# Optimization experiments

Hardware: AMD Instinct MI355X
Metric: run time of the kernel (lower is better)

## Reference

```python
import jax, jax.numpy as jnp
import numpy as np

ELU = jax.nn.elu
RELU = jax.nn.relu


def _mlp(x, W0, b0, Wh, bh, Wo, bo, act):
    # first hidden layer, stacked middle hidden layers, linear output layer
    h = act(x @ W0 + b0)
    for i in range(Wh.shape[0]):
        h = act(h @ Wh[i] + bh[i])
    return h @ Wo + bo


def _gru_layer(x_seq, h0, Wi, Wh, bi, bh):
    # torch nn.GRU gate math. x_seq: (T,B,I), h0: (B,H)
    xi = x_seq @ Wi.T + bi  # (T,B,3H) precomputed input projection

    def step(h, xt):
        hh = h @ Wh.T + bh
        xr, xz, xn = jnp.split(xt, 3, -1)
        hr, hz, hn = jnp.split(hh, 3, -1)
        r = jax.nn.sigmoid(xr + hr)
        z = jax.nn.sigmoid(xz + hz)
        n = jnp.tanh(xn + r * hn)
        hnew = (1.0 - z) * n + z * h
        return hnew, hnew

    hT, ys = jax.lax.scan(step, h0, xi)
    return ys, hT


def setup_inputs() -> dict:
    key = jax.random.key(0)
    ks = iter(jax.random.split(key, 64))
    B, T = 1024, 512
    S, SE, OE, GH = 4, 16, 16, 16
    OBJ_N, NULL_N, NOBJ = 3, 4, 7
    p = lambda *shape: jax.random.normal(next(ks), shape, jnp.float32) * 0.1
    return dict(
        envs=jax.random.normal(next(ks), (B, 9), jnp.float32),
        states=jax.random.normal(next(ks), (B, T, S), jnp.float32),
        # state embedder: 4 -> [16]*4 -> 16 (relu)
        se_W0=p(S, SE), se_b0=p(SE), se_Wh=p(3, SE, SE), se_bh=p(3, SE), se_Wo=p(SE, SE), se_bo=p(SE),
        # per-object embedders: 3 -> [16]*4 -> 16 (elu), stacked over 3 objects
        oe_W0=p(OBJ_N, 3, OE), oe_b0=p(OBJ_N, OE), oe_Wh=p(OBJ_N, 3, OE, OE), oe_bh=p(OBJ_N, 3, OE),
        oe_Wo=p(OBJ_N, OE, OE), oe_bo=p(OBJ_N, OE),
        null_embed=jax.random.uniform(next(ks), (NULL_N, OE), jnp.float32),
        init_gru_h=jax.random.uniform(next(ks), (2, GH), jnp.float32),
        # attention-score mlp: 32 -> [16]*3 -> 1 (elu)
        att_W0=p(SE + OE, 16), att_b0=p(16), att_Wh=p(2, 16, 16), att_bh=p(2, 16), att_Wo=p(16, 1), att_bo=p(1),
        # GRU: 2 layers, input 128, hidden 16
        gru0_Wi=p(3 * GH, SE + OE * NOBJ), gru0_Wh=p(3 * GH, GH), gru0_bi=p(3 * GH), gru0_bh=p(3 * GH),
        gru1_Wi=p(3 * GH, GH), gru1_Wh=p(3 * GH, GH), gru1_bi=p(3 * GH), gru1_bh=p(3 * GH),
        # relation MLPs: 32 -> [8]*2 -> 8 (elu), stacked over 7 slots
        rel_W0=p(NOBJ, GH + OE, 8), rel_b0=p(NOBJ, 8), rel_Wh=p(NOBJ, 1, 8, 8), rel_bh=p(NOBJ, 1, 8),
        rel_Wo=p(NOBJ, 8, 8), rel_bo=p(NOBJ, 8),
        # final mlp: 72 -> [4]*2 -> 4 (elu)
        fin_W0=p(GH + 8 * NOBJ, S), fin_b0=p(S), fin_Wh=p(1, S, S), fin_bh=p(1, S), fin_Wo=p(S, S), fin_bo=p(S),
        predict_t=0,
    )


def reference(envs, states, se_W0, se_b0, se_Wh, se_bh, se_Wo, se_bo,
              oe_W0, oe_b0, oe_Wh, oe_bh, oe_Wo, oe_bo,
              null_embed, init_gru_h,
              att_W0, att_b0, att_Wh, att_bh, att_Wo, att_bo,
              gru0_Wi, gru0_Wh, gru0_bi, gru0_bh, gru1_Wi, gru1_Wh, gru1_bi, gru1_bh,
              rel_W0, rel_b0, rel_Wh, rel_bh, rel_Wo, rel_bo,
              fin_W0, fin_b0, fin_Wh, fin_bh, fin_Wo, fin_bo,
              predict_t):
    B = envs.shape[0]
    T = states.shape[1]
    NOBJ = rel_W0.shape[0]  # 7 = obj_n + nullobj_n
    OE = null_embed.shape[1]

    # per-object embeddings: split envs into obj_n chunks, run per-slot MLPs (grouped via vmap)
    env_objs = envs.reshape(B, 3, 3).transpose(1, 0, 2)  # (3,B,3)
    obj_real = jax.vmap(lambda x, W0, b0, Wh, bh, Wo, bo: _mlp(x, W0, b0, Wh, bh, Wo, bo, ELU))(
        env_objs, oe_W0, oe_b0, oe_Wh, oe_bh, oe_Wo, oe_bo)  # (3,B,16)
    obj_null = jnp.broadcast_to(null_embed[:, None, :], (null_embed.shape[0], B, OE))  # (4,B,16)
    obj_embd = jnp.concatenate([obj_real, obj_null], 0)           # (7,B,16)
    obj_t = jnp.broadcast_to(obj_embd[:, None], (NOBJ, T, B, OE))  # (7,T,B,16)

    # state embedding over the full sequence (time-major like torch GRU)
    se = _mlp(states.transpose(1, 0, 2), se_W0, se_b0, se_Wh, se_bh, se_Wo, se_bo, RELU)  # (T,B,16)

    # attention scores per object slot
    def score_fn(emb):
        xin = jnp.concatenate([se, emb], -1)  # (T,B,32)
        return _mlp(xin, att_W0, att_b0, att_Wh, att_bh, att_Wo, att_bo, ELU)[..., 0]
    scores = jax.vmap(score_fn)(obj_t)  # (7,T,B)
    # PermuteLayer reverses the slot ordering before softmax over slots
    col_scores = jax.nn.softmax(jnp.flip(scores, 0), axis=0)  # (7,T,B)

    # GRU over [state_emb ; all obj embeds]
    gru_in = jnp.concatenate([se, jnp.moveaxis(obj_t, 0, 2).reshape(T, B, NOBJ * OE)], -1)  # (T,B,128)
    h0 = jnp.broadcast_to(init_gru_h[:, None, :], (2, B, init_gru_h.shape[1]))
    y0, _ = _gru_layer(gru_in, h0[0], gru0_Wi, gru0_Wh, gru0_bi, gru0_bh)
    gru_out, _ = _gru_layer(y0, h0[1], gru1_Wi, gru1_Wh, gru1_bi, gru1_bh)  # (T,B,16)

    # per-slot relation MLPs weighted by attention
    def rel_fn(emb, w, W0, b0, Wh, bh, Wo, bo):
        xin = jnp.concatenate([gru_out, emb], -1)  # (T,B,32)
        r = _mlp(xin, W0, b0, Wh, bh, Wo, bo, ELU)  # (T,B,8)
        return r * w[..., None]
    weighted = jax.vmap(rel_fn)(obj_t, col_scores, rel_W0, rel_b0, rel_Wh, rel_bh, rel_Wo, rel_bo)  # (7,T,B,8)

    final_in = jnp.concatenate([gru_out, jnp.moveaxis(weighted, 0, 2).reshape(T, B, -1)], -1)  # (T,B,72)
    out = _mlp(final_in, fin_W0, fin_b0, fin_Wh, fin_bh, fin_Wo, fin_bo, ELU)  # (T,B,4)
    return out.transpose(1, 0, 2)  # (B,T,4)
```

## Files before the change

kernel.cpp:

```cpp
#include <hip/hip_runtime.h>
#include <hip/hip_bf16.h>
#include <hip/hip_fp16.h>
#include <stdint.h>

#define TLEN 512
#define TCW 48
#define NCHK 11
__device__ __forceinline__ int csize(int i){ return (i == 10) ? 32 : 48; }

typedef unsigned short u16;
typedef unsigned int u32;

__device__ __forceinline__ float b2f(u16 u){ union{u32 i; float f;} v; v.i = ((u32)u)<<16; return v.f; }
__device__ __forceinline__ u16 f2bf(float f){
    union{float f; u32 i;} v; v.f = f;
    u32 b = v.i; b += 0x7fffu + ((b>>16)&1u);
    return (u16)(b>>16);
}
__device__ __forceinline__ float fexp2(float x){ return __builtin_amdgcn_exp2f(x); }
__device__ __forceinline__ float frcp(float x){ return __builtin_amdgcn_rcpf(x); }
#define LOG2E 1.4426950408889634f
__device__ __forceinline__ float elu_f(float x){ return x > 0.f ? x : fexp2(x*LOG2E) - 1.f; }
__device__ __forceinline__ float sigm(float x){ return frcp(1.f + fexp2(-LOG2E*x)); }
__device__ __forceinline__ float tanh_f(float x){ return 1.f - 2.f*frcp(1.f + fexp2((2.f*LOG2E)*x)); }

__device__ __forceinline__ float ldg(const void* p, int i, bool F){
    return F ? ((const float*)p)[i] : b2f(((const u16*)p)[i]);
}

__device__ void fill(float* dst, const void* src, int n, int tid, int nt, bool F){
    for (int i = tid; i < n; i += nt) dst[i] = ldg(src, i, F);
}
__device__ void fillS(float* dst, const void* src, int R, int C, int stride, int tid, int nt, bool F){
    for (int i = tid; i < R*C; i += nt){ int r = i / C, c = i % C; dst[i] = ldg(src, r*stride + c, F); }
}
__device__ void fillT(float* dst, const void* src, int K, int I, int stride, int tid, int nt, bool F){
    for (int idx = tid; idx < K*I; idx += nt){ int i = idx / K, k = idx % K; dst[idx] = ldg(src, k*stride + i, F); }
}

__global__ __launch_bounds__(256,1) void fused(
    const void* envs, const void* states,
    const void* se_W0, const void* se_b0, const void* se_Wh, const void* se_bh, const void* se_Wo, const void* se_bo,
    const void* oe_W0, const void* oe_b0, const void* oe_Wh, const void* oe_bh, const void* oe_Wo, const void* oe_bo,
    const void* null_embed, const void* init_h,
    const void* att_W0, const void* att_b0, const void* att_Wh, const void* att_bh, const void* att_Wo, const void* att_bo,
    const void* gru0_Wi, const void* gru0_Wh, const void* gru0_bi, const void* gru0_bh,
    const void* gru1_Wi, const void* gru1_Wh, const void* gru1_bi, const void* gru1_bh,
    const void* rel_W0, const void* rel_b0, const void* rel_Wh, const void* rel_bh, const void* rel_Wo, const void* rel_bo,
    const void* fin_W0, const void* fin_b0, const void* fin_Wh, const void* fin_bh, const void* fin_Wo, const void* fin_bo,
    void* out)
{
    __shared__ float sW0T[64], sb0[16], sWhT[768], sbh[48], sWoT[256], sbo[16];
    __shared__ float aW0T[256], aWhT[512], abh[32], aWo[16], abo_s[1];
    __shared__ float wi0se[768];
    __shared__ float rW0T[896], rWhT[448], rbh[56], rWoT[448], rbo[56];
    __shared__ float fW0T[288], fb0[4], fWhT[16], fbh[4], fWoT[16], fbo[4];
    __shared__ float E_att[448], E_rel[224], base_xi[192];
    __shared__ float gW0[768], gWi1[768], gWh1[768];
    __shared__ float g0bhn[16], g1bi48[48], g1bh48[48];
    __shared__ float scbuf[1728];
    __shared__ float uni[13632];
    __shared__ int s_isf32;

    const int tid = threadIdx.x, nt = 256;
    const int blk = blockIdx.x;
    const int wid = tid >> 6, ln = tid & 63;

    _Float16* bufA = (_Float16*)(uni);
    _Float16* bufB = (_Float16*)(uni + 4608);
    _Float16* gruA = (_Float16*)(uni + 9216);
    _Float16* gruB = (_Float16*)(uni + 10752);
    _Float16* cscA = (_Float16*)(uni + 12288);
    _Float16* cscB = (_Float16*)(uni + 12960);

    if (tid == 0){
        const u16* p = (const u16*)se_W0;
        int ok = 1;
        #pragma unroll
        for (int k = 0; k < 8; k++){
            float v = fabsf(b2f(p[2*k]));
            ok &= (v > 1e-12f && v < 16.f) ? 1 : 0;
        }
        s_isf32 = ok ? 0 : 1;
    }
    __syncthreads();
    const bool F = (s_isf32 != 0);

    fillT(sW0T, se_W0, 4, 16, 16, tid, nt, F);
    fill (sb0, se_b0, 16, tid, nt, F);
    for (int l = 0; l < 3; l++) fillT(sWhT + l*256, (const u16*)se_Wh + (F?l*512:l*256), 16, 16, 16, tid, nt, F);
    fill (sbh, se_bh, 48, tid, nt, F);
    fillT(sWoT, se_Wo, 16, 16, 16, tid, nt, F);
    fill (sbo, se_bo, 16, tid, nt, F);
    fillT(aW0T, att_W0, 16, 16, 16, tid, nt, F);
    for (int l = 0; l < 2; l++) fillT(aWhT + l*256, (const u16*)att_Wh + (F?l*512:l*256), 16, 16, 16, tid, nt, F);
    fill (abh, att_bh, 32, tid, nt, F);
    fill (aWo, att_Wo, 16, tid, nt, F);
    fill (abo_s, att_bo, 1, tid, nt, F);
    fillS(wi0se, gru0_Wi, 48, 16, 128, tid, nt, F);
    for (int s = 0; s < 7; s++){
        fillT(rW0T + s*128, (const u16*)rel_W0 + (F?s*512:s*256), 16, 8, 8, tid, nt, F);
        fillT(rWhT + s*64, (const u16*)rel_Wh + (F?s*128:s*64), 8, 8, 8, tid, nt, F);
        fillT(rWoT + s*64, (const u16*)rel_Wo + (F?s*128:s*64), 8, 8, 8, tid, nt, F);
    }
    fill (rbh, rel_bh, 56, tid, nt, F);
    fill (rbo, rel_bo, 56, tid, nt, F);
    fillT(fW0T, fin_W0, 72, 4, 4, tid, nt, F);
    fill (fb0, fin_b0, 4, tid, nt, F);
    fillT(fWhT, fin_Wh, 4, 4, 4, tid, nt, F);
    fill (fbh, fin_bh, 4, tid, nt, F);
    fillT(fWoT, fin_Wo, 4, 4, 4, tid, nt, F);
    fill (fbo, fin_bo, 4, tid, nt, F);
    fill (gW0,  gru0_Wh, 768, tid, nt, F);
    fill (gWi1, gru1_Wi, 768, tid, nt, F);
    fill (gWh1, gru1_Wh, 768, tid, nt, F);
    fill (g0bhn, (const u16*)gru0_bh + (F?64:32), 16, tid, nt, F);
    fill (g1bi48, gru1_bi, 48, tid, nt, F);
    fill (g1bh48, gru1_bh, 48, tid, nt, F);
    float* oeW0T = uni;
    float* oeb0  = uni + 144;
    float* oeWhT = uni + 192;
    float* oebh  = uni + 2496;
    float* oeWoT = uni + 2640;
    float* oebo  = uni + 3408;
    float* aW0To = uni + 3456;
    float* ab0   = uni + 3712;
    float* rW0To = uni + 3728;
    float* objE  = uni + 4624;
    for (int s = 0; s < 3; s++){
        fillT(oeW0T + s*48, (const u16*)oe_W0 + (F?s*96:s*48), 3, 16, 16, tid, nt, F);
        for (int l = 0; l < 3; l++)
            fillT(oeWhT + (s*3+l)*256, (const u16*)oe_Wh + (F?(s*3+l)*512:(s*3+l)*256), 16, 16, 16, tid, nt, F);
        fillT(oeWoT + s*256, (const u16*)oe_Wo + (F?s*512:s*256), 16, 16, 16, tid, nt, F);
    }
    fill(oeb0, oe_b0, 48, tid, nt, F);
    fill(oebh, oe_bh, 144, tid, nt, F);
    fill(oebo, oe_bo, 48, tid, nt, F);
    fillT(aW0To, (const u16*)att_W0 + (F?512:256), 16, 16, 16, tid, nt, F);
    fill (ab0, att_b0, 16, tid, nt, F);
    for (int s = 0; s < 7; s++)
        fillT(rW0To + s*128, (const u16*)rel_W0 + (F?(s*512+256):(s*256+128)), 16, 8, 8, tid, nt, F);
    __syncthreads();

    if (tid < 28){
        int b1 = tid / 7, s = tid % 7;
        float o[16];
        if (s < 3){
            int b = blk*4 + b1;
            float x0 = ldg(envs, b*9+3*s, F), x1 = ldg(envs, b*9+3*s+1, F), x2 = ldg(envs, b*9+3*s+2, F);
            float h[16], h2[16];
            #pragma unroll
            for (int i = 0; i < 16; i++){
                float a = oeb0[s*16+i] + x0*oeW0T[s*48+i*3] + x1*oeW0T[s*48+i*3+1] + x2*oeW0T[s*48+i*3+2];
                h[i] = elu_f(a);
            }
            for (int l = 0; l < 3; l++){
                #pragma unroll
                for (int i = 0; i < 16; i++){
                    float a = oebh[(s*3+l)*16+i];
                    #pragma unroll
                    for (int k = 0; k < 16; k++) a += h[k]*oeWhT[((s*3+l)*16+i)*16+k];
                    h2[i] = elu_f(a);
                }
                #pragma unroll
                for (int i = 0; i < 16; i++) h[i] = h2[i];
            }
            #pragma unroll
            for (int i = 0; i < 16; i++){
                float a = oebo[s*16+i];
                #pragma unroll
                for (int k = 0; k < 16; k++) a += h[k]*oeWoT[(s*16+i)*16+k];
                o[i] = a;
            }
        } else {
            #pragma unroll
            for (int i = 0; i < 16; i++) o[i] = ldg(null_embed, (s-3)*16 + i, F);
        }
        #pragma unroll
        for (int i = 0; i < 16; i++) objE[(b1*7+s)*16 + i] = o[i];
    }
    __syncthreads();

    for (int idx = tid; idx < 448; idx += nt){
        int r = idx % 112, i = r % 16;
        int os = (idx / 16) * 16;
        float a = ab0[i];
        #pragma unroll
        for (int k = 0; k < 16; k++) a += objE[os + k]*aW0To[i*16+k];
        E_att[idx] = a;
    }
    for (int idx = tid; idx < 224; idx += nt){
        int r = idx % 56, s = r / 8, i = r % 8;
        int b1 = idx / 56;
        float a = ldg(rel_b0, s*8+i, F);
        #pragma unroll
        for (int k = 0; k < 16; k++) a += objE[(b1*7+s)*16 + k]*rW0To[(s*8+i)*16+k];
        E_rel[idx] = a;
    }
    for (int idx = tid; idx < 192; idx += nt){
        int b1 = idx / 48, g = idx % 48;
        float a = ldg(gru0_bi, g, F) + (g < 32 ? ldg(gru0_bh, g, F) : 0.f);
        for (int s = 0; s < 7; s++){
            int wb = g*128 + 16 + s*16;
            #pragma unroll
            for (int k = 0; k < 16; k++) a += objE[(b1*7+s)*16 + k]*ldg(gru0_Wi, wb+k, F);
        }
        base_xi[idx] = a;
    }

    const int lj = ln & 15;
    const int gbase = ln & 48;
    float hp0 = 0.f, hp1 = 0.f;
    if (wid == 0){
        hp0 = ldg(init_h, lj, F);
        hp1 = ldg(init_h, 16 + lj, F);
    }
    const int mtid = tid - 64;
    const int b1p = (wid >= 1) ? (mtid / 48) : 0;
    const int tl  = (wid >= 1) ? (mtid % 48) : 0;
    const int bb  = blk*4 + b1p;
    __syncthreads();

    for (int c = 0; c <= NCHK+1; c++){
        if (wid == 0){
            if (c >= 1 && c <= NCHK){
                const int cs = c-1;
                const int tcs = csize(cs);
                const _Float16* xb = (cs&1) ? bufB : bufA;
                _Float16*       gb = (cs&1) ? gruB : gruA;
                float w0r[16], w0z[16], w0n[16], wi1r[16], wi1z[16], wi1n[16], wh1r[16], wh1z[16], wh1n[16];
                #pragma unroll
                for (int k = 0; k < 16; k++){
                    w0r[k]  = gW0[lj*16+k];  w0z[k]  = gW0[(16+lj)*16+k];  w0n[k]  = gW0[(32+lj)*16+k];
                    wi1r[k] = gWi1[lj*16+k]; wi1z[k] = gWi1[(16+lj)*16+k]; wi1n[k] = gWi1[(32+lj)*16+k];
                    wh1r[k] = gWh1[lj*16+k]; wh1z[k] = gWh1[(16+lj)*16+k]; wh1n[k] = gWh1[(32+lj)*16+k];
                }
                const float c0  = g0bhn[lj];
                const float cr  = g1bi48[lj]    + g1bh48[lj];
                const float cz  = g1bi48[16+lj] + g1bh48[16+lj];
                const float can = g1bi48[32+lj];
                const float cbn = g1bh48[32+lj];
                float h0[16], h1[16];
                #pragma unroll
                for (int k = 0; k < 16; k++){ h0[k] = __shfl(hp0, gbase + k); h1[k] = __shfl(hp1, gbase + k); }
                const int grp = ln >> 4;
                int sb = (grp*48 + 0)*48 + lj;
                float xr = (float)xb[sb], xz = (float)xb[sb+16], xn = (float)xb[sb+32];
                for (int s = 0; s < tcs; s++){
                    float xrn = 0.f, xzn = 0.f, xnn2 = 0.f;
                    if (s+1 < tcs){
                        int sb2 = (grp*48 + s+1)*48 + lj;
                        xrn = (float)xb[sb2]; xzn = (float)xb[sb2+16]; xnn2 = (float)xb[sb2+32];
                    }
                    float hr = 0.f, hz = 0.f, hn = c0;
                    #pragma unroll
                    for (int k = 0; k < 16; k++){ hr += h0[k]*w0r[k]; hz += h0[k]*w0z[k]; hn += h0[k]*w0n[k]; }
                    float r = sigm(xr + hr);
                    float z = sigm(xz + hz);
                    float n = tanh_f(xn + r*hn);
                    float h0n = (1.f - z)*n + z*hp0;
                    hp0 = h0n;
                    #pragma unroll
                    for (int k = 0; k < 16; k++) h0[k] = __shfl(h0n, gbase + k);
                    float ar = cr, az = cz, an = can, br = 0.f, bz = 0.f, bn = cbn;
                    #pragma unroll
                    for (int k = 0; k < 16; k++){
                        ar += h0[k]*wi1r[k]; az += h0[k]*wi1z[k]; an += h0[k]*wi1n[k];
                        br += h1[k]*wh1r[k]; bz += h1[k]*wh1z[k]; bn += h1[k]*wh1n[k];
                    }
                    float r1 = sigm(ar + br);
                    float z1 = sigm(az + bz);
                    float n1 = tanh_f(an + r1*bn);
                    float h1n = (1.f - z1)*n1 + z1*hp1;
                    hp1 = h1n;
                    gb[(grp*48 + s)*16 + lj] = (_Float16)h1n;
                    #pragma unroll
                    for (int k = 0; k < 16; k++) h1[k] = __shfl(h1n, gbase + k);
                    xr = xrn; xz = xzn; xn = xnn2;
                }
            }
        } else {
            if (c >= 2){
                const int cp = c-2;
                const int tcp = csize(cp);
                if (tl < tcp){
                    const _Float16* gb = (cp&1) ? gruB : gruA;
                    const _Float16* cb = (cp&1) ? cscB : cscA;
                    float g[16];
                    #pragma unroll
                    for (int i = 0; i < 16; i++) g[i] = (float)gb[(b1p*48 + tl)*16 + i];
                    float facc[4];
                    #pragma unroll
                    for (int cc = 0; cc < 4; cc++){
                        float a = fb0[cc];
                        #pragma unroll
                        for (int k = 0; k < 16; k++) a += g[k]*fW0T[cc*72+k];
                        facc[cc] = a;
                    }
                    #pragma unroll 1
                    for (int s = 0; s < 7; s++){
                        const float* ep = E_rel + (b1p*7+s)*8;
                        float p1a[8], p2a[8];
                        #pragma unroll
                        for (int i = 0; i < 8; i++){
                            float a = ep[i];
                            #pragma unroll
                            for (int k = 0; k < 16; k++) a += g[k]*rW0T[(s*8+i)*16+k];
                            p1a[i] = elu_f(a);
                        }
                        #pragma unroll
                        for (int i = 0; i < 8; i++){
                            float a = rbh[s*8+i];
                            #pragma unroll
                            for (int k = 0; k < 8; k++) a += p1a[k]*rWhT[(s*8+i)*8+k];
                            p2a[i] = elu_f(a);
                        }
                        float w = (float)cb[(b1p*7+s)*48 + tl];
                        #pragma unroll
                        for (int i = 0; i < 8; i++){
                            float a = rbo[s*8+i];
                            #pragma unroll
                            for (int k = 0; k < 8; k++) a += p2a[k]*rWoT[(s*8+i)*8+k];
                            float val = a*w;
                            #pragma unroll
                            for (int cc = 0; cc < 4; cc++) facc[cc] += val*fW0T[cc*72+16+s*8+i];
                        }
                    }
                    float f1[4], f2[4], o[4];
                    #pragma unroll
                    for (int cc = 0; cc < 4; cc++) f1[cc] = elu_f(facc[cc]);
                    #pragma unroll
                    for (int cc = 0; cc < 4; cc++){
                        float a = fbh[cc];
                        #pragma unroll
                        for (int k = 0; k < 4; k++) a += f1[k]*fWhT[cc*4+k];
                        f2[cc] = elu_f(a);
                    }
                    #pragma unroll
                    for (int cc = 0; cc < 4; cc++){
                        float a = fbo[cc];
                        #pragma unroll
                        for (int k = 0; k < 4; k++) a += f2[k]*fWoT[cc*4+k];
                        o[cc] = a;
                    }
                    size_t ofs = ((size_t)bb*TLEN + (cp*TCW + tl))*4;
                    if (F){
                        float4 v; v.x = o[0]; v.y = o[1]; v.z = o[2]; v.w = o[3];
                        *(float4*)((float*)out + ofs) = v;
                    } else {
                        u32 lo = (u32)f2bf(o[0]) | ((u32)f2bf(o[1]) << 16);
                        u32 hi = (u32)f2bf(o[2]) | ((u32)f2bf(o[3]) << 16);
                        *(uint2*)((u16*)out + ofs) = make_uint2(lo, hi);
                    }
                }
            }
            if (c < NCHK){
                const int tcc = csize(c);
                if (tl < tcc){
                    _Float16* xb = (c&1) ? bufB : bufA;
                    _Float16* cb = (c&1) ? cscB : cscA;
                    const int t = c*TCW + tl;
                    int sbase = ((int)bb*TLEN + t)*4;
                    float x0 = ldg(states, sbase+0, F), x1 = ldg(states, sbase+1, F);
                    float x2 = ldg(states, sbase+2, F), x3 = ldg(states, sbase+3, F);
                    float h[16], h2[16];
                    #pragma unroll
                    for (int i = 0; i < 16; i++){
                        float a = sb0[i] + x0*sW0T[i*4] + x1*sW0T[i*4+1] + x2*sW0T[i*4+2] + x3*sW0T[i*4+3];
                        h[i] = fmaxf(a, 0.f);
                    }
                    for (int l = 0; l < 3; l++){
                        #pragma unroll
                        for (int i = 0; i < 16; i++){
                            float a = sbh[l*16+i];
                            #pragma unroll
                            for (int k = 0; k < 16; k++) a += h[k]*sWhT[(l*16+i)*16+k];
                            h2[i] = fmaxf(a, 0.f);
                        }
                        #pragma unroll
                        for (int i = 0; i < 16; i++) h[i] = h2[i];
                    }
                    float se[16];
                    #pragma unroll
                    for (int i = 0; i < 16; i++){
                        float a = sbo[i];
                        #pragma unroll
                        for (int k = 0; k < 16; k++) a += h[k]*sWoT[i*16+k];
                        se[i] = a;
                    }
                    #pragma unroll 4
                    for (int g = 0; g < 48; g++){
                        float a = base_xi[b1p*48 + g];
                        #pragma unroll
                        for (int k = 0; k < 16; k++) a += se[k]*wi0se[g*16+k];
                        xb[(b1p*48 + tl)*48 + g] = (_Float16)a;
                    }
                    float satt[16];
                    #pragma unroll
                    for (int i = 0; i < 16; i++){
                        float a = 0.f;
                        #pragma unroll
                        for (int k = 0; k < 16; k++) a += se[k]*aW0T[i*16+k];
                        satt[i] = a;
                    }
                    const int mbase = (b1p*48 + tl)*9;
                    #pragma unroll 1
                    for (int s = 0; s < 7; s++){
                        const float* ep = E_att + (b1p*7+s)*16;
                        float a1[16], a2[16];
                        #pragma unroll
                        for (int i = 0; i < 16; i++) a1[i] = elu_f(satt[i] + ep[i]);
                        #pragma unroll
                        for (int i = 0; i < 16; i++){
                            float a = abh[i];
                            #pragma unroll
                            for (int k = 0; k < 16; k++) a += a1[k]*aWhT[i*16+k];
                            a2[i] = elu_f(a);
                        }
                        #pragma unroll
                        for (int i = 0; i < 16; i++){
                            float a = abh[16+i];
                            #pragma unroll
                            for (int k = 0; k < 16; k++) a += a2[k]*aWhT[256 + i*16+k];
                            a1[i] = elu_f(a);
                        }
                        float a = abo_s[0];
                        #pragma unroll
                        for (int k = 0; k < 16; k++) a += a1[k]*aWo[k];
                        scbuf[mbase + s] = a;
                    }
                    float sv[7];
                    #pragma unroll
                    for (int s = 0; s < 7; s++) sv[s] = scbuf[mbase + s];
                    float m = sv[0];
                    #pragma unroll
                    for (int s = 1; s < 7; s++) m = fmaxf(m, sv[s]);
                    float e[7], sum = 0.f;
                    #pragma unroll
                    for (int s = 0; s < 7; s++){ e[s] = fexp2((sv[s]-m)*LOG2E); sum += e[s]; }
                    float inv = frcp(sum);
                    #pragma unroll
                    for (int s = 0; s < 7; s++)
                        cb[(b1p*7+s)*48 + tl] = (_Float16)(e[6-s]*inv);
                }
            }
        }
        __syncthreads();
    }
}

extern "C" void kernel_launch(void* const* d_in, const int* in_sizes, int n_in,
                              void* d_out, int out_size, void* d_ws, size_t ws_size,
                              hipStream_t stream)
{
    (void)in_sizes; (void)n_in; (void)out_size; (void)d_ws; (void)ws_size;
    fused<<<dim3(256), dim3(256), 0, stream>>>(
        d_in[0],  d_in[1],
        d_in[2],  d_in[3],  d_in[4],  d_in[5],  d_in[6],  d_in[7],
        d_in[8],  d_in[9],  d_in[10], d_in[11], d_in[12], d_in[13],
        d_in[14], d_in[15],
        d_in[16], d_in[17], d_in[18], d_in[19], d_in[20], d_in[21],
        d_in[22], d_in[23], d_in[24], d_in[25],
        d_in[26], d_in[27], d_in[28], d_in[29],
        d_in[30], d_in[31], d_in[32], d_in[33], d_in[34], d_in[35],
        d_in[36], d_in[37], d_in[38], d_in[39], d_in[40], d_in[41],
        d_out);
}
```

Measured before the change: 886.6 us.

## Halve batch per block, widen time chunks, pair attention slots, defer softmax normalization

Each block now handles 2 batch rows instead of 4, and the grid doubles to 512 blocks so more CUs run the serial GRU recurrence concurrently. Time chunks grow from 48 to 80 steps, which cuts the number of pipeline stages. The attention MLP now evaluates two slots per iteration so weight loads are shared, and the softmax drops the max subtraction: it stores unnormalized exponentials plus a reciprocal sum that the consumer applies. Exponentials without max subtraction can overflow for large scores, and only 32 of 64 lanes in the GRU wave and 160 of 192 threads in the MLP waves do useful work.

New measurement: 1.886 ms. 2.13x slower.

```diff
diff --git a/kernel.cpp b/kernel.cpp
--- a/kernel.cpp
+++ b/kernel.cpp
@@ -4,9 +4,9 @@
 #include <stdint.h>
 
 #define TLEN 512
-#define TCW 48
-#define NCHK 11
-__device__ __forceinline__ int csize(int i){ return (i == 10) ? 32 : 48; }
+#define TCW 80
+#define NCHK 7
+__device__ __forceinline__ int csize(int i){ return (i == 6) ? 32 : 80; }
 
 typedef unsigned short u16;
 typedef unsigned int u32;
@@ -55,23 +55,24 @@
     __shared__ float wi0se[768];
     __shared__ float rW0T[896], rWhT[448], rbh[56], rWoT[448], rbo[56];
     __shared__ float fW0T[288], fb0[4], fWhT[16], fbh[4], fWoT[16], fbo[4];
-    __shared__ float E_att[448], E_rel[224], base_xi[192];
+    __shared__ float E_att[224], E_rel[112], base_xi[96];
     __shared__ float gW0[768], gWi1[768], gWh1[768];
     __shared__ float g0bhn[16], g1bi48[48], g1bh48[48];
-    __shared__ float scbuf[1728];
-    __shared__ float uni[13632];
+    __shared__ float uni[11680];
     __shared__ int s_isf32;
 
     const int tid = threadIdx.x, nt = 256;
     const int blk = blockIdx.x;
     const int wid = tid >> 6, ln = tid & 63;
 
-    _Float16* bufA = (_Float16*)(uni);
-    _Float16* bufB = (_Float16*)(uni + 4608);
-    _Float16* gruA = (_Float16*)(uni + 9216);
-    _Float16* gruB = (_Float16*)(uni + 10752);
-    _Float16* cscA = (_Float16*)(uni + 12288);
-    _Float16* cscB = (_Float16*)(uni + 12960);
+    _Float16* xiA  = (_Float16*)(uni);
+    _Float16* xiB  = (_Float16*)(uni + 3840);
+    _Float16* gruA = (_Float16*)(uni + 7680);
+    _Float16* gruB = (_Float16*)(uni + 8960);
+    _Float16* cscA = (_Float16*)(uni + 10240);
+    _Float16* cscB = (_Float16*)(uni + 10800);
+    float*    invA = uni + 11360;
+    float*    invB = uni + 11520;
 
     if (tid == 0){
         const u16* p = (const u16*)se_W0;
@@ -142,11 +143,11 @@
         fillT(rW0To + s*128, (const u16*)rel_W0 + (F?(s*512+256):(s*256+128)), 16, 8, 8, tid, nt, F);
     __syncthreads();
 
-    if (tid < 28){
+    if (tid < 14){
         int b1 = tid / 7, s = tid % 7;
         float o[16];
         if (s < 3){
-            int b = blk*4 + b1;
+            int b = blk*2 + b1;
             float x0 = ldg(envs, b*9+3*s, F), x1 = ldg(envs, b*9+3*s+1, F), x2 = ldg(envs, b*9+3*s+2, F);
             float h[16], h2[16];
             #pragma unroll
@@ -181,7 +182,7 @@
     }
     __syncthreads();
 
-    for (int idx = tid; idx < 448; idx += nt){
+    for (int idx = tid; idx < 224; idx += nt){
         int r = idx % 112, i = r % 16;
         int os = (idx / 16) * 16;
         float a = ab0[i];
@@ -189,7 +190,7 @@
         for (int k = 0; k < 16; k++) a += objE[os + k]*aW0To[i*16+k];
         E_att[idx] = a;
     }
-    for (int idx = tid; idx < 224; idx += nt){
+    for (int idx = tid; idx < 112; idx += nt){
         int r = idx % 56, s = r / 8, i = r % 8;
         int b1 = idx / 56;
         float a = ldg(rel_b0, s*8+i, F);
@@ -197,7 +198,7 @@
         for (int k = 0; k < 16; k++) a += objE[(b1*7+s)*16 + k]*rW0To[(s*8+i)*16+k];
         E_rel[idx] = a;
     }
-    for (int idx = tid; idx < 192; idx += nt){
+    for (int idx = tid; idx < 96; idx += nt){
         int b1 = idx / 48, g = idx % 48;
         float a = ldg(gru0_bi, g, F) + (g < 32 ? ldg(gru0_bh, g, F) : 0.f);
         for (int s = 0; s < 7; s++){
@@ -211,22 +212,23 @@
     const int lj = ln & 15;
     const int gbase = ln & 48;
     float hp0 = 0.f, hp1 = 0.f;
-    if (wid == 0){
+    if (wid == 0 && ln < 32){
         hp0 = ldg(init_h, lj, F);
         hp1 = ldg(init_h, 16 + lj, F);
     }
     const int mtid = tid - 64;
-    const int b1p = (wid >= 1) ? (mtid / 48) : 0;
-    const int tl  = (wid >= 1) ? (mtid % 48) : 0;
-    const int bb  = blk*4 + b1p;
+    const bool mact = (wid >= 1) && (mtid < 160);
+    const int b1p = mact ? (mtid / 80) : 0;
+    const int tl  = mact ? (mtid % 80) : 0;
+    const int bb  = blk*2 + b1p;
     __syncthreads();
 
     for (int c = 0; c <= NCHK+1; c++){
         if (wid == 0){
-            if (c >= 1 && c <= NCHK){
+            if (ln < 32 && c >= 1 && c <= NCHK){
                 const int cs = c-1;
                 const int tcs = csize(cs);
-                const _Float16* xb = (cs&1) ? bufB : bufA;
+                const _Float16* xb = (cs&1) ? xiB : xiA;
                 _Float16*       gb = (cs&1) ? gruB : gruA;
                 float w0r[16], w0z[16], w0n[16], wi1r[16], wi1z[16], wi1n[16], wh1r[16], wh1z[16], wh1n[16];
                 #pragma unroll
@@ -244,12 +246,12 @@
                 #pragma unroll
                 for (int k = 0; k < 16; k++){ h0[k] = __shfl(hp0, gbase + k); h1[k] = __shfl(hp1, gbase + k); }
                 const int grp = ln >> 4;
-                int sb = (grp*48 + 0)*48 + lj;
+                int sb = (grp*80 + 0)*48 + lj;
                 float xr = (float)xb[sb], xz = (float)xb[sb+16], xn = (float)xb[sb+32];
                 for (int s = 0; s < tcs; s++){
                     float xrn = 0.f, xzn = 0.f, xnn2 = 0.f;
                     if (s+1 < tcs){
-                        int sb2 = (grp*48 + s+1)*48 + lj;
+                        int sb2 = (grp*80 + s+1)*48 + lj;
                         xrn = (float)xb[sb2]; xzn = (float)xb[sb2+16]; xnn2 = (float)xb[sb2+32];
                     }
                     float hr = 0.f, hz = 0.f, hn = c0;
@@ -273,22 +275,23 @@
                     float n1 = tanh_f(an + r1*bn);
                     float h1n = (1.f - z1)*n1 + z1*hp1;
                     hp1 = h1n;
-                    gb[(grp*48 + s)*16 + lj] = (_Float16)h1n;
+                    gb[(grp*80 + s)*16 + lj] = (_Float16)h1n;
                     #pragma unroll
                     for (int k = 0; k < 16; k++) h1[k] = __shfl(h1n, gbase + k);
                     xr = xrn; xz = xzn; xn = xnn2;
                 }
             }
-        } else {
+        } else if (mact) {
             if (c >= 2){
                 const int cp = c-2;
                 const int tcp = csize(cp);
                 if (tl < tcp){
                     const _Float16* gb = (cp&1) ? gruB : gruA;
                     const _Float16* cb = (cp&1) ? cscB : cscA;
+                    const float invv = ((cp&1) ? invB : invA)[b1p*80 + tl];
                     float g[16];
                     #pragma unroll
-                    for (int i = 0; i < 16; i++) g[i] = (float)gb[(b1p*48 + tl)*16 + i];
+                    for (int i = 0; i < 16; i++) g[i] = (float)gb[(b1p*80 + tl)*16 + i];
                     float facc[4];
                     #pragma unroll
                     for (int cc = 0; cc < 4; cc++){
@@ -315,7 +318,7 @@
                             for (int k = 0; k < 8; k++) a += p1a[k]*rWhT[(s*8+i)*8+k];
                             p2a[i] = elu_f(a);
                         }
-                        float w = (float)cb[(b1p*7+s)*48 + tl];
+                        float w = (float)cb[(b1p*7+s)*80 + tl] * invv;
                         #pragma unroll
                         for (int i = 0; i < 8; i++){
                             float a = rbo[s*8+i];
@@ -357,8 +360,9 @@
             if (c < NCHK){
                 const int tcc = csize(c);
                 if (tl < tcc){
-                    _Float16* xb = (c&1) ? bufB : bufA;
+                    _Float16* xb = (c&1) ? xiB : xiA;
                     _Float16* cb = (c&1) ? cscB : cscA;
+                    float*   ivb = (c&1) ? invB : invA;
                     const int t = c*TCW + tl;
                     int sbase = ((int)bb*TLEN + t)*4;
                     float x0 = ldg(states, sbase+0, F), x1 = ldg(states, sbase+1, F);
@@ -393,7 +397,7 @@
                         float a = base_xi[b1p*48 + g];
                         #pragma unroll
                         for (int k = 0; k < 16; k++) a += se[k]*wi0se[g*16+k];
-                        xb[(b1p*48 + tl)*48 + g] = (_Float16)a;
+                        xb[(b1p*80 + tl)*48 + g] = (_Float16)a;
                     }
                     float satt[16];
                     #pragma unroll
@@ -403,45 +407,54 @@
                         for (int k = 0; k < 16; k++) a += se[k]*aW0T[i*16+k];
                         satt[i] = a;
                     }
-                    const int mbase = (b1p*48 + tl)*9;
+                    float sum = 0.f;
                     #pragma unroll 1
-                    for (int s = 0; s < 7; s++){
-                        const float* ep = E_att + (b1p*7+s)*16;
-                        float a1[16], a2[16];
-                        #pragma unroll
-                        for (int i = 0; i < 16; i++) a1[i] = elu_f(satt[i] + ep[i]);
+                    for (int s = 0; s < 7; s += 2){
+                        const bool two = (s < 6);
+                        const float* epx = E_att + (b1p*7+s)*16;
+                        const float* epy = E_att + (b1p*7+(two ? s+1 : s))*16;
+                        float a1x[16], a1y[16], a2x[16], a2y[16];
                         #pragma unroll
                         for (int i = 0; i < 16; i++){
-                            float a = abh[i];
-                            #pragma unroll
-                            for (int k = 0; k < 16; k++) a += a1[k]*aWhT[i*16+k];
-                            a2[i] = elu_f(a);
+                            a1x[i] = elu_f(satt[i] + epx[i]);
+                            a1y[i] = elu_f(satt[i] + epy[i]);
                         }
                         #pragma unroll
                         for (int i = 0; i < 16; i++){
-                            float a = abh[16+i];
-                            #pragma unroll
-                            for (int k = 0; k < 16; k++) a += a2[k]*aWhT[256 + i*16+k];
-                            a1[i] = elu_f(a);
-                        }
-                        float a = abo_s[0];
-                        #pragma unroll
-                        for (int k = 0; k < 16; k++) a += a1[k]*aWo[k];
-                        scbuf[mbase + s] = a;
-                    }
-                    float sv[7];
-                    #pragma unroll
-                    for (int s = 0; s < 7; s++) sv[s] = scbuf[mbase + s];
-                    float m = sv[0];
-                    #pragma unroll
-                    for (int s = 1; s < 7; s++) m = fmaxf(m, sv[s]);
-                    float e[7], sum = 0.f;
-                    #pragma unroll
-                    for (int s = 0; s < 7; s++){ e[s] = fexp2((sv[s]-m)*LOG2E); sum += e[s]; }
-                    float inv = frcp(sum);
-                    #pragma unroll
-                    for (int s = 0; s < 7; s++)
-                        cb[(b1p*7+s)*48 + tl] = (_Float16)(e[6-s]*inv);
+                            float ax = abh[i], ay = abh[i];
+                            #pragma unroll
+                            for (int k = 0; k < 16; k++){
+                                float w = aWhT[i*16+k];
+                                ax += a1x[k]*w; ay += a1y[k]*w;
+                            }
+                            a2x[i] = elu_f(ax); a2y[i] = elu_f(ay);
+                        }
+                        #pragma unroll
+                        for (int i = 0; i < 16; i++){
+                            float ax = abh[16+i], ay = abh[16+i];
+                            #pragma unroll
+                            for (int k = 0; k < 16; k++){
+                                float w = aWhT[256 + i*16+k];
+                                ax += a2x[k]*w; ay += a2y[k]*w;
+                            }
+                            a1x[i] = elu_f(ax); a1y[i] = elu_f(ay);
+                        }
+                        float scx = abo_s[0], scy = abo_s[0];
+                        #pragma unroll
+                        for (int k = 0; k < 16; k++){
+                            float w = aWo[k];
+                            scx += a1x[k]*w; scy += a1y[k]*w;
+                        }
+                        float ex = fexp2(scx*LOG2E);
+                        cb[(b1p*7+(6-s))*80 + tl] = (_Float16)ex;
+                        sum += ex;
+                        if (two){
+                            float ey = fexp2(scy*LOG2E);
+                            cb[(b1p*7+(5-s))*80 + tl] = (_Float16)ey;
+                            sum += ey;
+                        }
+                    }
+                    ivb[b1p*80 + tl] = frcp(sum);
                 }
             }
         }
@@ -454,7 +467,7 @@
                               hipStream_t stream)
 {
     (void)in_sizes; (void)n_in; (void)out_size; (void)d_ws; (void)ws_size;
-    fused<<<dim3(256), dim3(256), 0, stream>>>(
+    fused<<<dim3(512), dim3(256), 0, stream>>>(
         d_in[0],  d_in[1],
         d_in[2],  d_in[3],  d_in[4],  d_in[5],  d_in[6],  d_in[7],
         d_in[8],  d_in[9],  d_in[10], d_in[11], d_in[12], d_in[13],
```

## Drop GRU weight LDS copies and defer softmax normalization to consumer

Applied to the files above, without the earlier changes.

GRU weights are no longer staged in shared memory; the GRU wave loads them from global memory straight into registers once per chunk. The attention softmax no longer goes through a scratch buffer with a max subtraction. Each slot's exp score is written directly as fp16 along with a per-timestep reciprocal sum, and the relation stage applies that reciprocal. This frees a large amount of LDS and removes a pass over the scores. The risk is that dropping the max subtraction can overflow fp16 when scores are large.

Measured after the change: 911.7 us. +2.8%, slower.

```diff
diff --git a/kernel.cpp b/kernel.cpp
--- a/kernel.cpp
+++ b/kernel.cpp
@@ -56,10 +56,8 @@
     __shared__ float rW0T[896], rWhT[448], rbh[56], rWoT[448], rbo[56];
     __shared__ float fW0T[288], fb0[4], fWhT[16], fbh[4], fWoT[16], fbo[4];
     __shared__ float E_att[448], E_rel[224], base_xi[192];
-    __shared__ float gW0[768], gWi1[768], gWh1[768];
     __shared__ float g0bhn[16], g1bi48[48], g1bh48[48];
-    __shared__ float scbuf[1728];
-    __shared__ float uni[13632];
+    __shared__ float uni[14016];
     __shared__ int s_isf32;
 
     const int tid = threadIdx.x, nt = 256;
@@ -72,6 +70,8 @@
     _Float16* gruB = (_Float16*)(uni + 10752);
     _Float16* cscA = (_Float16*)(uni + 12288);
     _Float16* cscB = (_Float16*)(uni + 12960);
+    float*    invA = uni + 13632;
+    float*    invB = uni + 13824;
 
     if (tid == 0){
         const u16* p = (const u16*)se_W0;
@@ -111,9 +111,6 @@
     fill (fbh, fin_bh, 4, tid, nt, F);
     fillT(fWoT, fin_Wo, 4, 4, 4, tid, nt, F);
     fill (fbo, fin_bo, 4, tid, nt, F);
-    fill (gW0,  gru0_Wh, 768, tid, nt, F);
-    fill (gWi1, gru1_Wi, 768, tid, nt, F);
-    fill (gWh1, gru1_Wh, 768, tid, nt, F);
     fill (g0bhn, (const u16*)gru0_bh + (F?64:32), 16, tid, nt, F);
     fill (g1bi48, gru1_bi, 48, tid, nt, F);
     fill (g1bh48, gru1_bh, 48, tid, nt, F);
@@ -231,9 +228,15 @@
                 float w0r[16], w0z[16], w0n[16], wi1r[16], wi1z[16], wi1n[16], wh1r[16], wh1z[16], wh1n[16];
                 #pragma unroll
                 for (int k = 0; k < 16; k++){
-                    w0r[k]  = gW0[lj*16+k];  w0z[k]  = gW0[(16+lj)*16+k];  w0n[k]  = gW0[(32+lj)*16+k];
-                    wi1r[k] = gWi1[lj*16+k]; wi1z[k] = gWi1[(16+lj)*16+k]; wi1n[k] = gWi1[(32+lj)*16+k];
-                    wh1r[k] = gWh1[lj*16+k]; wh1z[k] = gWh1[(16+lj)*16+k]; wh1n[k] = gWh1[(32+lj)*16+k];
+                    w0r[k]  = ldg(gru0_Wh, lj*16+k, F);
+                    w0z[k]  = ldg(gru0_Wh, (16+lj)*16+k, F);
+                    w0n[k]  = ldg(gru0_Wh, (32+lj)*16+k, F);
+                    wi1r[k] = ldg(gru1_Wi, lj*16+k, F);
+                    wi1z[k] = ldg(gru1_Wi, (16+lj)*16+k, F);
+                    wi1n[k] = ldg(gru1_Wi, (32+lj)*16+k, F);
+                    wh1r[k] = ldg(gru1_Wh, lj*16+k, F);
+                    wh1z[k] = ldg(gru1_Wh, (16+lj)*16+k, F);
+                    wh1n[k] = ldg(gru1_Wh, (32+lj)*16+k, F);
                 }
                 const float c0  = g0bhn[lj];
                 const float cr  = g1bi48[lj]    + g1bh48[lj];
@@ -286,6 +289,7 @@
                 if (tl < tcp){
                     const _Float16* gb = (cp&1) ? gruB : gruA;
                     const _Float16* cb = (cp&1) ? cscB : cscA;
+                    const float invv = ((cp&1) ? invB : invA)[b1p*48 + tl];
                     float g[16];
                     #pragma unroll
                     for (int i = 0; i < 16; i++) g[i] = (float)gb[(b1p*48 + tl)*16 + i];
@@ -315,7 +319,7 @@
                             for (int k = 0; k < 8; k++) a += p1a[k]*rWhT[(s*8+i)*8+k];
                             p2a[i] = elu_f(a);
                         }
-                        float w = (float)cb[(b1p*7+s)*48 + tl];
+                        float w = (float)cb[(b1p*7+s)*48 + tl] * invv;
                         #pragma unroll
                         for (int i = 0; i < 8; i++){
                             float a = rbo[s*8+i];
@@ -359,6 +363,7 @@
                 if (tl < tcc){
                     _Float16* xb = (c&1) ? bufB : bufA;
                     _Float16* cb = (c&1) ? cscB : cscA;
+                    float*   ivb = (c&1) ? invB : invA;
                     const int t = c*TCW + tl;
                     int sbase = ((int)bb*TLEN + t)*4;
                     float x0 = ldg(states, sbase+0, F), x1 = ldg(states, sbase+1, F);
@@ -403,7 +408,7 @@
                         for (int k = 0; k < 16; k++) a += se[k]*aW0T[i*16+k];
                         satt[i] = a;
                     }
-                    const int mbase = (b1p*48 + tl)*9;
+                    float sum = 0.f;
                     #pragma unroll 1
                     for (int s = 0; s < 7; s++){
                         const float* ep = E_att + (b1p*7+s)*16;
@@ -427,21 +432,11 @@
                         float a = abo_s[0];
                         #pragma unroll
                         for (int k = 0; k < 16; k++) a += a1[k]*aWo[k];
-                        scbuf[mbase + s] = a;
-                    }
-                    float sv[7];
-                    #pragma unroll
-                    for (int s = 0; s < 7; s++) sv[s] = scbuf[mbase + s];
-                    float m = sv[0];
-                    #pragma unroll
-                    for (int s = 1; s < 7; s++) m = fmaxf(m, sv[s]);
-                    float e[7], sum = 0.f;
-                    #pragma unroll
-                    for (int s = 0; s < 7; s++){ e[s] = fexp2((sv[s]-m)*LOG2E); sum += e[s]; }
-                    float inv = frcp(sum);
-                    #pragma unroll
-                    for (int s = 0; s < 7; s++)
-                        cb[(b1p*7+s)*48 + tl] = (_Float16)(e[6-s]*inv);
+                        float ex = fexp2(a*LOG2E);
+                        cb[(b1p*7+(6-s))*48 + tl] = (_Float16)ex;
+                        sum += ex;
+                    }
+                    ivb[b1p*48 + tl] = frcp(sum);
                 }
             }
         }
```
